# Kernel optimization log

Hardware: AMD Instinct MI355X
Metric: run time of the kernel (lower is better)

## Reference

```python
import jax, jax.numpy as jnp
import numpy as np

D_MODEL = 1024
NUM_HEADS = 16
HEAD_SIZE = D_MODEL // NUM_HEADS
ROPE_BASE = 10000.0
RMS_EPS = 1e-6


def rms_norm(x, scale):
    # torchtune RMSNorm: fp32 compute, eps=1e-6, learned scale
    xf = x.astype(jnp.float32)
    n = xf * jax.lax.rsqrt(jnp.mean(xf * xf, axis=-1, keepdims=True) + RMS_EPS)
    return (n * scale).astype(x.dtype)


def rope(x):
    # torchtune RotaryPositionalEmbeddings: interleaved pairs. x: [B,T,H,hd]
    B, T, H, hd = x.shape
    half = hd // 2
    theta = 1.0 / (ROPE_BASE ** (jnp.arange(0, hd, 2, dtype=jnp.float32) / hd))  # [half]
    ang = jnp.arange(T, dtype=jnp.float32)[:, None] * theta[None, :]  # [T,half]
    cos = jnp.cos(ang)[None, :, None, :]  # [1,T,1,half]
    sin = jnp.sin(ang)[None, :, None, :]
    xs = x.reshape(B, T, H, half, 2)
    x0, x1 = xs[..., 0], xs[..., 1]
    out = jnp.stack([x0 * cos - x1 * sin, x1 * cos + x0 * sin], axis=-1)
    return out.reshape(B, T, H, hd).astype(x.dtype)


def setup_inputs() -> dict:
    key = jax.random.key(0)
    ks = jax.random.split(key, 10)
    s = 0.02
    D = D_MODEL
    return {
        "x": jax.random.normal(ks[0], (2, 2048, D), dtype=jnp.float32),
        "rms_scale": jnp.ones((D,), dtype=jnp.float32),
        "in_proj_w": jax.random.normal(ks[1], (3 * D, D), dtype=jnp.float32) * s,
        "in_proj_b": jnp.zeros((3 * D,), dtype=jnp.float32),
        "out_proj_w": jax.random.normal(ks[2], (D, D), dtype=jnp.float32) * s,
        "out_proj_b": jnp.zeros((D,), dtype=jnp.float32),
        "w1": jax.random.normal(ks[3], (4 * D, D), dtype=jnp.float32) * s,
        "b1": jnp.zeros((4 * D,), dtype=jnp.float32),
        "w2": jax.random.normal(ks[4], (D, 4 * D), dtype=jnp.float32) * s,
        "b2": jnp.zeros((D,), dtype=jnp.float32),
    }


def reference(x, rms_scale, in_proj_w, in_proj_b, out_proj_w, out_proj_b, w1, b1, w2, b2):
    B, T, D = x.shape
    H, hd = NUM_HEADS, HEAD_SIZE

    xn = rms_norm(x, rms_scale)
    # RoPE on pre-projection q/k (as in original module), value = xn
    q_in = rope(xn.reshape(B, T, H, hd)).reshape(B, T, D)
    k_in = rope(xn.reshape(B, T, H, hd)).reshape(B, T, D)
    v_in = xn

    Wq, Wk, Wv = jnp.split(in_proj_w, 3, axis=0)
    bq, bk, bv = jnp.split(in_proj_b, 3, axis=0)
    q = (q_in @ Wq.T + bq).reshape(B, T, H, hd).transpose(0, 2, 1, 3)  # [B,H,T,hd]
    k = (k_in @ Wk.T + bk).reshape(B, T, H, hd).transpose(0, 2, 1, 3)
    v = (v_in @ Wv.T + bv).reshape(B, T, H, hd).transpose(0, 2, 1, 3)

    scores = jnp.einsum('bhqd,bhkd->bhqk', q, k) / jnp.sqrt(jnp.float32(hd))
    causal = jnp.tril(jnp.ones((T, T), dtype=bool))  # True = keep
    scores = jnp.where(causal[None, None], scores, jnp.float32(-1e30))
    attn = jax.nn.softmax(scores, axis=-1)
    ctx = jnp.einsum('bhqk,bhkd->bhqd', attn, v)  # [B,H,T,hd]
    attn_out = ctx.transpose(0, 2, 1, 3).reshape(B, T, D) @ out_proj_w.T + out_proj_b

    # NOTE: original overwrites x with attention output (no residual on attention)
    y = attn_out
    yn = rms_norm(y, rms_scale)
    ffn = jax.nn.silu(yn @ w1.T + b1) @ w2.T + b2
    return y + ffn
```

## Files before the change

### kernel.cpp

```cpp
#include <hip/hip_runtime.h>
#include <math.h>
#include <stdint.h>

#define D_MODEL 1024
#define NUM_HEADS 16
#define HEAD_SIZE 64
#define SEQ_T 2048

typedef __bf16 bf16;
typedef __bf16 bf16x8 __attribute__((ext_vector_type(8)));
typedef float f32x4 __attribute__((ext_vector_type(4)));

__device__ __forceinline__ void gld_lds16(const bf16* g, bf16* l) {
    __builtin_amdgcn_global_load_lds(
        (__attribute__((address_space(1))) void*)(const_cast<bf16*>(g)),
        (__attribute__((address_space(3))) void*)(l), 16, 0, 0);
}

struct __align__(8) b4pack { bf16 v[4]; };

__global__ __launch_bounds__(256) void cast_all_weights(const float* __restrict__ s0, bf16* __restrict__ d0, int n0,
                                                        const float* __restrict__ s1, bf16* __restrict__ d1, int n1,
                                                        const float* __restrict__ s2, bf16* __restrict__ d2, int n2,
                                                        const float* __restrict__ s3, bf16* __restrict__ d3, int n3) {
    int i = (blockIdx.x * 256 + threadIdx.x) * 4;
    const float* src;
    bf16* dst;
    if (i < n0) { src = s0; dst = d0; }
    else if (i < n0 + n1) { i -= n0; src = s1; dst = d1; }
    else if (i < n0 + n1 + n2) { i -= n0 + n1; src = s2; dst = d2; }
    else { i -= n0 + n1 + n2; if (i >= n3) return; src = s3; dst = d3; }
    float4 v = *(const float4*)(src + i);
    b4pack o;
    o.v[0] = (bf16)v.x; o.v[1] = (bf16)v.y; o.v[2] = (bf16)v.z; o.v[3] = (bf16)v.w;
    *(b4pack*)(dst + i) = o;
}

__global__ __launch_bounds__(256) void rmsnorm_rope_kernel(const float* __restrict__ x,
                                                           const float* __restrict__ scale,
                                                           bf16* __restrict__ xn,
                                                           bf16* __restrict__ rp, int T) {
    __shared__ float red[4];
    int row = blockIdx.x;
    int t = row % T;
    const float* xp = x + (size_t)row * D_MODEL;
    int tid = threadIdx.x;
    float4 xv = *(const float4*)(xp + tid * 4);
    float s = xv.x * xv.x + xv.y * xv.y + xv.z * xv.z + xv.w * xv.w;
    for (int off = 32; off; off >>= 1) s += __shfl_down(s, off);
    if ((tid & 63) == 0) red[tid >> 6] = s;
    __syncthreads();
    if (tid == 0) red[0] = red[0] + red[1] + red[2] + red[3];
    __syncthreads();
    float inv = rsqrtf(red[0] * (1.0f / D_MODEL) + 1e-6f);
    float4 sc = *(const float4*)(scale + tid * 4);
    float n0 = xv.x * inv * sc.x, n1 = xv.y * inv * sc.y;
    float n2 = xv.z * inv * sc.z, n3 = xv.w * inv * sc.w;
    b4pack pn;
    pn.v[0] = (bf16)n0; pn.v[1] = (bf16)n1; pn.v[2] = (bf16)n2; pn.v[3] = (bf16)n3;
    *(b4pack*)(xn + (size_t)row * D_MODEL + tid * 4) = pn;
    int p0 = 2 * tid;
    float th0 = expf(-0.2878231366242557f * (float)(p0 & 31));
    float th1 = expf(-0.2878231366242557f * (float)((p0 + 1) & 31));
    float s0, c0, s1, c1;
    sincosf((float)t * th0, &s0, &c0);
    sincosf((float)t * th1, &s1, &c1);
    b4pack pr;
    pr.v[0] = (bf16)(n0 * c0 - n1 * s0);
    pr.v[1] = (bf16)(n1 * c0 + n0 * s0);
    pr.v[2] = (bf16)(n2 * c1 - n3 * s1);
    pr.v[3] = (bf16)(n3 * c1 + n2 * s1);
    *(b4pack*)(rp + (size_t)row * D_MODEL + tid * 4) = pr;
}

__global__ __launch_bounds__(256) void rmsnorm_kernel(const float* __restrict__ x,
                                                      const float* __restrict__ scale,
                                                      bf16* __restrict__ out) {
    __shared__ float red[4];
    int row = blockIdx.x;
    const float* xp = x + (size_t)row * D_MODEL;
    bf16* op = out + (size_t)row * D_MODEL;
    int tid = threadIdx.x;
    float s = 0.f;
    for (int i = tid; i < D_MODEL; i += 256) { float v = xp[i]; s += v * v; }
    for (int off = 32; off; off >>= 1) s += __shfl_down(s, off);
    if ((tid & 63) == 0) red[tid >> 6] = s;
    __syncthreads();
    if (tid == 0) red[0] = red[0] + red[1] + red[2] + red[3];
    __syncthreads();
    float inv = rsqrtf(red[0] * (1.0f / D_MODEL) + 1e-6f);
    for (int i = tid; i < D_MODEL; i += 256) op[i] = (bf16)(xp[i] * inv * scale[i]);
}

template <int ACT, int ADD, int OUT_BF16, int VT>
__global__ __launch_bounds__(256) void gemm_bf16(const bf16* __restrict__ A,
                                                 const bf16* __restrict__ A2, int splitN,
                                                 const bf16* __restrict__ W,
                                                 const float* __restrict__ bias,
                                                 float* __restrict__ Cf,
                                                 bf16* __restrict__ Cb,
                                                 bf16* __restrict__ Vtp, int Tlen,
                                                 int M, int N, int K) {
    __shared__ __align__(16) bf16 As[128 * 32];
    __shared__ __align__(16) bf16 Bs[128 * 32];
    int tid = threadIdx.x;
    int m0 = blockIdx.y * 128, n0 = blockIdx.x * 128;
    const bf16* Ag = (n0 < splitN) ? A : A2;

    int lane = tid & 63, w = tid >> 6;
    int wm = w >> 1, wn = w & 1;
    int lm = lane & 15, quad = lane >> 4;

    int c0 = tid, c1 = tid + 256;
    int ar0 = c0 >> 2, ak0 = (c0 & 3) * 8;
    int ar1 = c1 >> 2, ak1 = (c1 & 3) * 8;

    f32x4 acc[4][4];
#pragma unroll
    for (int i = 0; i < 4; i++)
#pragma unroll
        for (int j = 0; j < 4; j++)
#pragma unroll
            for (int r = 0; r < 4; r++) acc[i][j][r] = 0.f;

    int abase = (wm * 64 + lm) * 32 + quad * 8;
    int bbase = (wn * 64 + lm) * 32 + quad * 8;

    for (int k0 = 0; k0 < K; k0 += 32) {
        __syncthreads();
        gld_lds16(Ag + (size_t)(m0 + ar0) * K + k0 + ak0, As + c0 * 8);
        gld_lds16(Ag + (size_t)(m0 + ar1) * K + k0 + ak1, As + c1 * 8);
        gld_lds16(W  + (size_t)(n0 + ar0) * K + k0 + ak0, Bs + c0 * 8);
        gld_lds16(W  + (size_t)(n0 + ar1) * K + k0 + ak1, Bs + c1 * 8);
        __syncthreads();
        bf16x8 af[4], bfr[4];
#pragma unroll
        for (int i = 0; i < 4; i++) af[i] = *(const bf16x8*)&As[abase + i * 16 * 32];
#pragma unroll
        for (int j = 0; j < 4; j++) bfr[j] = *(const bf16x8*)&Bs[bbase + j * 16 * 32];
#pragma unroll
        for (int i = 0; i < 4; i++)
#pragma unroll
            for (int j = 0; j < 4; j++)
                acc[i][j] = __builtin_amdgcn_mfma_f32_16x16x32_bf16(af[i], bfr[j], acc[i][j], 0, 0, 0);
    }

    if (VT && n0 >= 2 * D_MODEL) {
#pragma unroll
        for (int j = 0; j < 4; j++) {
            int col = n0 + wn * 64 + j * 16 + lm;
            int dimg = col - 2 * D_MODEL;
            float bv = bias[col];
#pragma unroll
            for (int i = 0; i < 4; i++) {
                int row0 = m0 + wm * 64 + i * 16 + quad * 4;
                int bb = row0 / Tlen, t0 = row0 % Tlen;
                b4pack pk;
#pragma unroll
                for (int r = 0; r < 4; r++) pk.v[r] = (bf16)(acc[i][j][r] + bv);
                *(b4pack*)(Vtp + ((size_t)bb * D_MODEL + dimg) * Tlen + t0) = pk;
            }
        }
        return;
    }

#pragma unroll
    for (int j = 0; j < 4; j++) {
        int col = n0 + wn * 64 + j * 16 + lm;
        float bv = bias[col];
#pragma unroll
        for (int i = 0; i < 4; i++) {
#pragma unroll
            for (int r = 0; r < 4; r++) {
                int row = m0 + wm * 64 + i * 16 + quad * 4 + r;
                float v = acc[i][j][r] + bv;
                if (ACT == 1) v = v / (1.f + __expf(-v));
                size_t idx = (size_t)row * N + col;
                if (ADD) v += Cf[idx];
                if (OUT_BF16) Cb[idx] = (bf16)v;
                else Cf[idx] = v;
            }
        }
    }
}

template <int ADD>
__global__ __launch_bounds__(256) void gemm_bf16_skinny2(const bf16* __restrict__ A,
                                                         const bf16* __restrict__ W,
                                                         const float* __restrict__ bias,
                                                         float* __restrict__ Cf,
                                                         int M, int N, int K) {
    __shared__ __align__(16) bf16 As[2][64 * 64];
    __shared__ __align__(16) bf16 Bs[2][128 * 64];
    int tid = threadIdx.x;

    int nblk = gridDim.x;
    int q = nblk >> 3;
    int swz = (blockIdx.x & 7) * q + (blockIdx.x >> 3);
    int nb = swz & 7;
    int mb = swz >> 3;
    int m0 = mb * 64, n0 = nb * 128;

    int lane = tid & 63, w = tid >> 6;
    int wm = w >> 1, wn = w & 1;
    int lm = lane & 15, quad = lane >> 4;
    int lm7 = lm & 7;

    int ar0 = tid >> 3, ac0 = (tid & 7) ^ (ar0 & 7);
    int t1 = tid + 256;
    int ar1 = t1 >> 3, ac1 = (t1 & 7) ^ (ar1 & 7);

    f32x4 acc[2][4];
#pragma unroll
    for (int i = 0; i < 2; i++)
#pragma unroll
        for (int j = 0; j < 4; j++)
#pragma unroll
            for (int r = 0; r < 4; r++) acc[i][j][r] = 0.f;

    int nt = K >> 6;

    {
        gld_lds16(A + (size_t)(m0 + ar0) * K + ac0 * 8, &As[0][0] + tid * 8);
        gld_lds16(A + (size_t)(m0 + ar1) * K + ac1 * 8, &As[0][0] + t1 * 8);
#pragma unroll
        for (int i = 0; i < 4; i++) {
            int c = tid + 256 * i;
            int r = c >> 3, cc = (c & 7) ^ (r & 7);
            gld_lds16(W + (size_t)(n0 + r) * K + cc * 8, &Bs[0][0] + c * 8);
        }
    }

    for (int t = 0; t < nt; ++t) {
        int cur = t & 1;
        if (t + 1 < nt) {
            int k0 = (t + 1) << 6;
            bf16* as = &As[cur ^ 1][0];
            bf16* bs = &Bs[cur ^ 1][0];
            gld_lds16(A + (size_t)(m0 + ar0) * K + k0 + ac0 * 8, as + tid * 8);
            gld_lds16(A + (size_t)(m0 + ar1) * K + k0 + ac1 * 8, as + t1 * 8);
#pragma unroll
            for (int i = 0; i < 4; i++) {
                int c = tid + 256 * i;
                int r = c >> 3, cc = (c & 7) ^ (r & 7);
                gld_lds16(W + (size_t)(n0 + r) * K + k0 + cc * 8, bs + c * 8);
            }
            asm volatile("s_waitcnt vmcnt(6)" ::: "memory");
        } else {
            asm volatile("s_waitcnt vmcnt(0)" ::: "memory");
        }
        __builtin_amdgcn_s_barrier();

        const bf16* as = &As[cur][0];
        const bf16* bs = &Bs[cur][0];
        bf16x8 af[2][2], bfr[4][2];
#pragma unroll
        for (int i = 0; i < 2; i++) {
            int row = wm * 32 + i * 16 + lm;
#pragma unroll
            for (int h = 0; h < 2; h++)
                af[i][h] = *(const bf16x8*)&as[row * 64 + ((h * 4 + quad) ^ lm7) * 8];
        }
#pragma unroll
        for (int j = 0; j < 4; j++) {
            int row = wn * 64 + j * 16 + lm;
#pragma unroll
            for (int h = 0; h < 2; h++)
                bfr[j][h] = *(const bf16x8*)&bs[row * 64 + ((h * 4 + quad) ^ lm7) * 8];
        }
#pragma unroll
        for (int i = 0; i < 2; i++)
#pragma unroll
            for (int j = 0; j < 4; j++) {
                acc[i][j] = __builtin_amdgcn_mfma_f32_16x16x32_bf16(af[i][0], bfr[j][0], acc[i][j], 0, 0, 0);
                acc[i][j] = __builtin_amdgcn_mfma_f32_16x16x32_bf16(af[i][1], bfr[j][1], acc[i][j], 0, 0, 0);
            }
        asm volatile("" ::: "memory");
        __builtin_amdgcn_s_barrier();
    }

#pragma unroll
    for (int j = 0; j < 4; j++) {
        int col = n0 + wn * 64 + j * 16 + lm;
        float bv = bias[col];
#pragma unroll
        for (int i = 0; i < 2; i++) {
#pragma unroll
            for (int r = 0; r < 4; r++) {
                int row = m0 + wm * 32 + i * 16 + quad * 4 + r;
                float v = acc[i][j][r] + bv;
                size_t idx = (size_t)row * N + col;
                if (ADD) v += Cf[idx];
                Cf[idx] = v;
            }
        }
    }
}

__global__ __launch_bounds__(256, 2) void attn_mfma_kernel(const bf16* __restrict__ QKV,
                                                           const bf16* __restrict__ Vt,
                                                           bf16* __restrict__ Og, int T) {
    __shared__ __align__(16) bf16 Ks[2][2][64 * 64];
    __shared__ __align__(16) bf16 Vs[2][2][64 * 64];
    __shared__ __align__(16) bf16 Ps[4 * 16 * 64];
    const int ldq = 3 * D_MODEL;
    int bidx = blockIdx.x;
    int c = bidx & 7;
    int rest = bidx >> 3;
    int p = rest & 15;
    int bhoct = rest >> 4;
    int bh = bhoct * 8 + c;
    int qtA = 31 - p, qtB = p;
    int h = bh & (NUM_HEADS - 1), b = bh / NUM_HEADS;
    int tid = threadIdx.x;
    int w = tid >> 6, lane = tid & 63;
    int lm = lane & 15, quad = lane >> 4;
    int qrowA = qtA * 64 + w * 16, qrowB = qtB * 64 + w * 16;

    int s0 = tid, s1 = tid + 256;
    int sr0 = s0 >> 3, sc0 = (s0 & 7) ^ (sr0 & 7);
    int sr1 = s1 >> 3, sc1 = (s1 & 7) ^ (sr1 & 7);

    const bf16* QpA = QKV + ((size_t)(b * T + qrowA + lm)) * ldq + h * HEAD_SIZE + quad * 8;
    bf16x8 qfA0 = *(const bf16x8*)QpA;
    bf16x8 qfA1 = *(const bf16x8*)(QpA + 32);
    const bf16* QpB = QKV + ((size_t)(b * T + qrowB + lm)) * ldq + h * HEAD_SIZE + quad * 8;
    bf16x8 qfB0 = *(const bf16x8*)QpB;
    bf16x8 qfB1 = *(const bf16x8*)(QpB + 32);

    const bf16* Kbase = QKV + ((size_t)b * T) * ldq + D_MODEL + h * HEAD_SIZE;
    const bf16* Vbase = Vt + ((size_t)b * D_MODEL + h * HEAD_SIZE) * T;
    const float C = 0.1803368801111204f;
    bf16* PsW = Ps + w * 16 * 64;
    int lm7 = lm & 7;

    bf16x8 ones;
#pragma unroll
    for (int i = 0; i < 8; i++) ones[i] = (bf16)1.0f;

    f32x4 oA[4], oB[4], laccA, laccB;
#pragma unroll
    for (int r = 0; r < 4; r++) {
        oA[r] = (f32x4){0.f, 0.f, 0.f, 0.f};
        oB[r] = (f32x4){0.f, 0.f, 0.f, 0.f};
        laccA[r] = 0.f; laccB[r] = 0.f;
    }

    int nktA = (qtA + 2) >> 1;
    int nktB = (qtB + 2) >> 1;

    auto stage = [&](int buf, int k0) {
        gld_lds16(Kbase + (size_t)(k0 + sr0) * ldq + sc0 * 8, &Ks[buf][0][0] + s0 * 8);
        gld_lds16(Kbase + (size_t)(k0 + sr1) * ldq + sc1 * 8, &Ks[buf][0][0] + s1 * 8);
        gld_lds16(Kbase + (size_t)(k0 + 64 + sr0) * ldq + sc0 * 8, &Ks[buf][1][0] + s0 * 8);
        gld_lds16(Kbase + (size_t)(k0 + 64 + sr1) * ldq + sc1 * 8, &Ks[buf][1][0] + s1 * 8);
        gld_lds16(Vbase + (size_t)sr0 * T + k0 + sc0 * 8, &Vs[buf][0][0] + s0 * 8);
        gld_lds16(Vbase + (size_t)sr1 * T + k0 + sc1 * 8, &Vs[buf][0][0] + s1 * 8);
        gld_lds16(Vbase + (size_t)sr0 * T + k0 + 64 + sc0 * 8, &Vs[buf][1][0] + s0 * 8);
        gld_lds16(Vbase + (size_t)sr1 * T + k0 + 64 + sc1 * 8, &Vs[buf][1][0] + s1 * 8);
    };

    auto run_tile = [&](int cur, int k0, bf16x8 qf0, bf16x8 qf1, int qrow0,
                        f32x4 (&o)[4], f32x4& lacc, bool lastmask) {
        f32x4 sa[2][4];
        __builtin_amdgcn_s_setprio(1);
#pragma unroll
        for (int u = 0; u < 2; u++) {
            const bf16* Ksu = &Ks[cur][u][0];
#pragma unroll
            for (int jb = 0; jb < 4; jb++) {
                int n = jb * 16 + lm;
                bf16x8 kf0 = *(const bf16x8*)&Ksu[(n * 8 + (quad ^ lm7)) * 8];
                bf16x8 kf1 = *(const bf16x8*)&Ksu[(n * 8 + ((quad + 4) ^ lm7)) * 8];
                f32x4 a = {0.f, 0.f, 0.f, 0.f};
                a = __builtin_amdgcn_mfma_f32_16x16x32_bf16(qf0, kf0, a, 0, 0, 0);
                a = __builtin_amdgcn_mfma_f32_16x16x32_bf16(qf1, kf1, a, 0, 0, 0);
                sa[u][jb] = a;
            }
        }
        __builtin_amdgcn_s_setprio(0);
        if (lastmask) {
#pragma unroll
            for (int u = 0; u < 2; u++)
#pragma unroll
                for (int jb = 0; jb < 4; jb++)
#pragma unroll
                    for (int r = 0; r < 4; r++)
                        if (k0 + u * 64 + jb * 16 + lm > qrow0 + quad * 4 + r)
                            sa[u][jb][r] = -3.0e38f;
        }
#pragma unroll
        for (int u = 0; u < 2; u++) {
            const bf16* Vsu = &Vs[cur][u][0];
#pragma unroll
            for (int jb = 0; jb < 4; jb++) {
                int g = jb * 2 + (lm >> 3);
#pragma unroll
                for (int r = 0; r < 4; r++) {
                    int row = quad * 4 + r;
                    float pv = exp2f(sa[u][jb][r] * C);
                    PsW[row * 64 + ((g ^ (row & 7)) * 8) + lm7] = (bf16)pv;
                }
            }
            bf16x8 pf0 = *(const bf16x8*)&PsW[lm * 64 + ((quad ^ lm7) * 8)];
            bf16x8 pf1 = *(const bf16x8*)&PsW[lm * 64 + (((quad + 4) ^ lm7) * 8)];
            __builtin_amdgcn_s_setprio(1);
#pragma unroll
            for (int db = 0; db < 4; db++) {
                int n = db * 16 + lm;
                bf16x8 vf0 = *(const bf16x8*)&Vsu[(n * 8 + (quad ^ lm7)) * 8];
                bf16x8 vf1 = *(const bf16x8*)&Vsu[(n * 8 + ((quad + 4) ^ lm7)) * 8];
                o[db] = __builtin_amdgcn_mfma_f32_16x16x32_bf16(pf0, vf0, o[db], 0, 0, 0);
                o[db] = __builtin_amdgcn_mfma_f32_16x16x32_bf16(pf1, vf1, o[db], 0, 0, 0);
            }
            lacc = __builtin_amdgcn_mfma_f32_16x16x32_bf16(pf0, ones, lacc, 0, 0, 0);
            lacc = __builtin_amdgcn_mfma_f32_16x16x32_bf16(pf1, ones, lacc, 0, 0, 0);
            __builtin_amdgcn_s_setprio(0);
        }
    };

    stage(0, 0);
    for (int kt = 0; kt < nktA; kt++) {
        int cur = kt & 1;
        if (kt + 1 < nktA) {
            stage(cur ^ 1, (kt + 1) * 128);
            asm volatile("s_waitcnt vmcnt(8)" ::: "memory");
        } else {
            asm volatile("s_waitcnt vmcnt(0)" ::: "memory");
        }
        __builtin_amdgcn_s_barrier();
        asm volatile("" ::: "memory");
        int k0 = kt * 128;
        run_tile(cur, k0, qfA0, qfA1, qrowA, oA, laccA, kt == nktA - 1);
        if (kt < nktB)
            run_tile(cur, k0, qfB0, qfB1, qrowB, oB, laccB, kt == nktB - 1);
        asm volatile("" ::: "memory");
        __builtin_amdgcn_s_barrier();
    }

    {
        float inv[4];
#pragma unroll
        for (int r = 0; r < 4; r++) inv[r] = 1.f / laccA[r];
        bf16* Ob = Og + ((size_t)(b * T + qrowA + quad * 4)) * D_MODEL + h * HEAD_SIZE + lm;
#pragma unroll
        for (int r = 0; r < 4; r++)
#pragma unroll
            for (int db = 0; db < 4; db++)
                Ob[(size_t)r * D_MODEL + db * 16] = (bf16)(oA[db][r] * inv[r]);
    }
    {
        float inv[4];
#pragma unroll
        for (int r = 0; r < 4; r++) inv[r] = 1.f / laccB[r];
        bf16* Ob = Og + ((size_t)(b * T + qrowB + quad * 4)) * D_MODEL + h * HEAD_SIZE + lm;
#pragma unroll
        for (int r = 0; r < 4; r++)
#pragma unroll
            for (int db = 0; db < 4; db++)
                Ob[(size_t)r * D_MODEL + db * 16] = (bf16)(oB[db][r] * inv[r]);
    }
}

extern "C" void kernel_launch(void* const* d_in, const int* in_sizes, int n_in,
                              void* d_out, int out_size, void* d_ws, size_t ws_size,
                              hipStream_t stream) {
    const float* x          = (const float*)d_in[0];
    const float* rms_scale  = (const float*)d_in[1];
    const float* in_proj_w  = (const float*)d_in[2];
    const float* in_proj_b  = (const float*)d_in[3];
    const float* out_proj_w = (const float*)d_in[4];
    const float* out_proj_b = (const float*)d_in[5];
    const float* w1         = (const float*)d_in[6];
    const float* b1         = (const float*)d_in[7];
    const float* w2         = (const float*)d_in[8];
    const float* b2         = (const float*)d_in[9];
    float* out = (float*)d_out;

    const int rows = in_sizes[0] / D_MODEL;
    const int T = SEQ_T;
    const int B = rows / T;
    const int D = D_MODEL;

    bf16* inwb  = (bf16*)d_ws;
    bf16* outwb = inwb + (size_t)3 * D * D;
    bf16* w1b   = outwb + (size_t)D * D;
    bf16* w2b   = w1b + (size_t)4 * D * D;
    bf16* XNb   = w2b + (size_t)4 * D * D;
    bf16* RPb   = XNb + (size_t)rows * D;
    bf16* QKV   = RPb + (size_t)rows * D;
    bf16* Vt    = QKV + (size_t)rows * 3 * D;
    bf16* CTXb  = XNb;
    bf16* YNb   = RPb;
    bf16* H1b   = QKV;

    {
        int n0 = 3 * D * D, n1 = D * D, n2 = 4 * D * D, n3 = 4 * D * D;
        int tot4 = (n0 + n1 + n2 + n3) / 4;
        cast_all_weights<<<(tot4 + 255) / 256, 256, 0, stream>>>(
            in_proj_w, inwb, n0, out_proj_w, outwb, n1, w1, w1b, n2, w2, w2b, n3);
    }
    rmsnorm_rope_kernel<<<rows, 256, 0, stream>>>(x, rms_scale, XNb, RPb, T);
    {
        dim3 g(3 * D / 128, rows / 128);
        gemm_bf16<0, 0, 1, 1><<<g, 256, 0, stream>>>(RPb, XNb, 2 * D, inwb, in_proj_b,
                                                     nullptr, QKV, Vt, T, rows, 3 * D, D);
    }
    attn_mfma_kernel<<<B * NUM_HEADS * (T / 128), 256, 0, stream>>>(QKV, Vt, CTXb, T);
    {
        int nblk = (D / 128) * (rows / 64);
        gemm_bf16_skinny2<0><<<nblk, 256, 0, stream>>>(CTXb, outwb, out_proj_b, out,
                                                       rows, D, D);
    }
    rmsnorm_kernel<<<rows, 256, 0, stream>>>(out, rms_scale, YNb);
    {
        dim3 g(4 * D / 128, rows / 128);
        gemm_bf16<1, 0, 1, 0><<<g, 256, 0, stream>>>(YNb, YNb, 4 * D, w1b, b1,
                                                     nullptr, H1b, nullptr, 1, rows, 4 * D, D);
    }
    {
        int nblk = (D / 128) * (rows / 64);
        gemm_bf16_skinny2<1><<<nblk, 256, 0, stream>>>(H1b, w2b, b2, out,
                                                       rows, D, 4 * D);
    }
}
```

Measured before the change: 359.8 us.

## Double-buffer GEMM LDS tiles with BK=64 and XOR-swizzled layout

Restructures the bf16 GEMM main loop to prefetch the next K-tile into a second LDS buffer while computing on the current one, using manual vmcnt waits and raw barriers. The K tile is widened from 32 to 64 so there are fewer barriers per unit of work, and the LDS layout is XOR-swizzled so fragment reads avoid bank conflicts. This doubles-plus the LDS footprint to 64KB per block, which may lower occupancy, and the hand-written waitcnt logic carries correctness risk.

```diff
diff --git a/kernel.cpp b/kernel.cpp
--- a/kernel.cpp
+++ b/kernel.cpp
@@ -101,8 +101,8 @@
                                                  bf16* __restrict__ Cb,
                                                  bf16* __restrict__ Vtp, int Tlen,
                                                  int M, int N, int K) {
-    __shared__ __align__(16) bf16 As[128 * 32];
-    __shared__ __align__(16) bf16 Bs[128 * 32];
+    __shared__ __align__(16) bf16 As[2][128 * 64];
+    __shared__ __align__(16) bf16 Bs[2][128 * 64];
     int tid = threadIdx.x;
     int m0 = blockIdx.y * 128, n0 = blockIdx.x * 128;
     const bf16* Ag = (n0 < splitN) ? A : A2;
@@ -110,10 +110,7 @@
     int lane = tid & 63, w = tid >> 6;
     int wm = w >> 1, wn = w & 1;
     int lm = lane & 15, quad = lane >> 4;
-
-    int c0 = tid, c1 = tid + 256;
-    int ar0 = c0 >> 2, ak0 = (c0 & 3) * 8;
-    int ar1 = c1 >> 2, ak1 = (c1 & 3) * 8;
+    int lm7 = lm & 7;
 
     f32x4 acc[4][4];
 #pragma unroll
@@ -123,26 +120,61 @@
 #pragma unroll
             for (int r = 0; r < 4; r++) acc[i][j][r] = 0.f;
 
-    int abase = (wm * 64 + lm) * 32 + quad * 8;
-    int bbase = (wn * 64 + lm) * 32 + quad * 8;
-
-    for (int k0 = 0; k0 < K; k0 += 32) {
-        __syncthreads();
-        gld_lds16(Ag + (size_t)(m0 + ar0) * K + k0 + ak0, As + c0 * 8);
-        gld_lds16(Ag + (size_t)(m0 + ar1) * K + k0 + ak1, As + c1 * 8);
-        gld_lds16(W  + (size_t)(n0 + ar0) * K + k0 + ak0, Bs + c0 * 8);
-        gld_lds16(W  + (size_t)(n0 + ar1) * K + k0 + ak1, Bs + c1 * 8);
-        __syncthreads();
-        bf16x8 af[4], bfr[4];
-#pragma unroll
-        for (int i = 0; i < 4; i++) af[i] = *(const bf16x8*)&As[abase + i * 16 * 32];
-#pragma unroll
-        for (int j = 0; j < 4; j++) bfr[j] = *(const bf16x8*)&Bs[bbase + j * 16 * 32];
+    int nt = K >> 6;
+
+#pragma unroll
+    for (int i = 0; i < 4; i++) {
+        int cch = tid + 256 * i;
+        int r = cch >> 3, cc = (cch & 7) ^ (r & 7);
+        gld_lds16(Ag + (size_t)(m0 + r) * K + cc * 8, &As[0][0] + cch * 8);
+        gld_lds16(W  + (size_t)(n0 + r) * K + cc * 8, &Bs[0][0] + cch * 8);
+    }
+
+    for (int t = 0; t < nt; ++t) {
+        int cur = t & 1;
+        if (t + 1 < nt) {
+            int k0 = (t + 1) << 6;
+            bf16* as = &As[cur ^ 1][0];
+            bf16* bs = &Bs[cur ^ 1][0];
+#pragma unroll
+            for (int i = 0; i < 4; i++) {
+                int cch = tid + 256 * i;
+                int r = cch >> 3, cc = (cch & 7) ^ (r & 7);
+                gld_lds16(Ag + (size_t)(m0 + r) * K + k0 + cc * 8, as + cch * 8);
+                gld_lds16(W  + (size_t)(n0 + r) * K + k0 + cc * 8, bs + cch * 8);
+            }
+            asm volatile("s_waitcnt vmcnt(8)" ::: "memory");
+        } else {
+            asm volatile("s_waitcnt vmcnt(0)" ::: "memory");
+        }
+        __builtin_amdgcn_s_barrier();
+
+        const bf16* as = &As[cur][0];
+        const bf16* bs = &Bs[cur][0];
+        bf16x8 af[4][2], bfr[4][2];
+#pragma unroll
+        for (int i = 0; i < 4; i++) {
+            int row = wm * 64 + i * 16 + lm;
+#pragma unroll
+            for (int h2 = 0; h2 < 2; h2++)
+                af[i][h2] = *(const bf16x8*)&as[row * 64 + ((h2 * 4 + quad) ^ lm7) * 8];
+        }
+#pragma unroll
+        for (int j = 0; j < 4; j++) {
+            int row = wn * 64 + j * 16 + lm;
+#pragma unroll
+            for (int h2 = 0; h2 < 2; h2++)
+                bfr[j][h2] = *(const bf16x8*)&bs[row * 64 + ((h2 * 4 + quad) ^ lm7) * 8];
+        }
 #pragma unroll
         for (int i = 0; i < 4; i++)
 #pragma unroll
-            for (int j = 0; j < 4; j++)
-                acc[i][j] = __builtin_amdgcn_mfma_f32_16x16x32_bf16(af[i], bfr[j], acc[i][j], 0, 0, 0);
+            for (int j = 0; j < 4; j++) {
+                acc[i][j] = __builtin_amdgcn_mfma_f32_16x16x32_bf16(af[i][0], bfr[j][0], acc[i][j], 0, 0, 0);
+                acc[i][j] = __builtin_amdgcn_mfma_f32_16x16x32_bf16(af[i][1], bfr[j][1], acc[i][j], 0, 0, 0);
+            }
+        asm volatile("" ::: "memory");
+        __builtin_amdgcn_s_barrier();
     }
 
     if (VT && n0 >= 2 * D_MODEL) {
```

Result: faster. 332.8 us (-7.5%).
